# Kernel tuning notes

Measured on AMD Instinct MI355X. Metric: run time of the kernel, lower is better.

Reference implementation:

```python
import jax, jax.numpy as jnp
import numpy as np

N_EMBD = 768
HIDDEN = 4 * N_EMBD
N_EXPERTS = 8
TOP_K = 2


def setup_inputs() -> dict:
    key = jax.random.key(0)
    ks = jax.random.split(key, 4)
    B, T, C, E, H = 4, 2048, N_EMBD, N_EXPERTS, HIDDEN
    x = jax.random.normal(ks[0], (B, T, C), dtype=jnp.float32)
    gate_w = jax.random.normal(ks[1], (E, C), dtype=jnp.float32) * 0.02
    gate_b = jnp.zeros((E,), dtype=jnp.float32)
    w_fc = jax.random.normal(ks[2], (E, H, C), dtype=jnp.float32) * 0.02
    b_fc = jnp.zeros((E, H), dtype=jnp.float32)
    w_proj = jax.random.normal(ks[3], (E, C, H), dtype=jnp.float32) * 0.02
    b_proj = jnp.zeros((E, C), dtype=jnp.float32)
    return {"x": x, "gate_w": gate_w, "gate_b": gate_b, "w_fc": w_fc,
            "b_fc": b_fc, "w_proj": w_proj, "b_proj": b_proj}


def reference(x, gate_w, gate_b, w_fc, b_fc, w_proj, b_proj):
    B, T, C = x.shape
    E = gate_b.shape[0]
    xf = x.reshape(-1, C)  # [N, C]
    # gating: Linear(C -> E), top-k, softmax over the k selected scores
    scores = xf @ gate_w.T + gate_b                      # [N, E]
    top_s, top_i = jax.lax.top_k(scores, TOP_K)          # [N, K]
    gates = jax.nn.softmax(top_s, axis=-1)               # [N, K]
    # combine weight per (token, expert): sum_k gate[t,k] * 1[top_i[t,k]==e]
    comb = jnp.sum(jax.nn.one_hot(top_i, E, dtype=xf.dtype) * gates[..., None], axis=1)  # [N, E]
    out = jnp.zeros_like(xf)
    for j in range(E):  # loop over fixed small expert count
        h = jax.nn.gelu(xf @ w_fc[j].T + b_fc[j], approximate=True)  # [N, H]
        y = h @ w_proj[j].T + b_proj[j]                              # [N, C]
        out = out + comb[:, j:j + 1] * y
    return out.reshape(B, T, C)
```

## Files before the change

kernel.cpp:

```cpp
#include <hip/hip_runtime.h>
#include <cmath>

#define N_TOK 8192
#define C_DIM 768
#define H_DIM 3072
#define NEXP  8
#define PADCAP 18432

typedef short short8 __attribute__((ext_vector_type(8)));
typedef unsigned short ushort8 __attribute__((ext_vector_type(8)));
typedef float f32x4  __attribute__((ext_vector_type(4)));

__device__ __forceinline__ unsigned short f2b(float f) {
  unsigned int u = __float_as_uint(f);
  u += 0x7fffu + ((u >> 16) & 1u);
  return (unsigned short)(u >> 16);
}
__device__ __forceinline__ float b2f(unsigned short u) {
  return __uint_as_float((unsigned int)u << 16);
}
__device__ __forceinline__ void gll(const char* g, char* l) {
  __builtin_amdgcn_global_load_lds((const __attribute__((address_space(1))) void*)g,
                                   (__attribute__((address_space(3))) void*)l, 16, 0, 0);
}

__global__ __launch_bounds__(256) void gate_kernel(
    const float* __restrict__ x, const float* __restrict__ gw,
    const float* __restrict__ gb, int* __restrict__ counts,
    int* __restrict__ tok_e, int* __restrict__ tok_r, float* __restrict__ tok_w) {
  __shared__ float gwl[NEXP * C_DIM];
  __shared__ double red[256][NEXP];
  int tid = threadIdx.x;
  const float4* gw4 = (const float4*)gw;
  float4* gl4 = (float4*)gwl;
  for (int i = tid; i < NEXP * C_DIM / 4; i += 256) gl4[i] = gw4[i];
  __syncthreads();
  int tl = tid & 63;
  int kc = tid >> 6;
  int t = blockIdx.x * 64 + tl;
  double acc[NEXP];
#pragma unroll
  for (int e = 0; e < NEXP; e++) acc[e] = 0.0;
  const float* xr = x + (size_t)t * C_DIM;
  for (int k = kc * 192; k < kc * 192 + 192; k++) {
    double xv = (double)xr[k];
#pragma unroll
    for (int e = 0; e < NEXP; e++) acc[e] += xv * (double)gwl[e * C_DIM + k];
  }
#pragma unroll
  for (int e = 0; e < NEXP; e++) red[tid][e] = acc[e];
  __syncthreads();
  if (tid < 64) {
    double s[NEXP];
#pragma unroll
    for (int e = 0; e < NEXP; e++)
      s[e] = (double)gb[e] + red[tid][e] + red[tid + 64][e] + red[tid + 128][e] + red[tid + 192][e];
    double best = s[0], sec = -1e300; int bi = 0, si = -1;
#pragma unroll
    for (int e = 1; e < NEXP; e++) {
      if (s[e] > best)      { sec = best; si = bi; best = s[e]; bi = e; }
      else if (s[e] > sec)  { sec = s[e]; si = e; }
    }
    double ex = exp(sec - best);
    double den = 1.0 + ex;
    tok_e[2 * t] = bi;  tok_e[2 * t + 1] = si;
    tok_w[2 * t] = (float)(1.0 / den);  tok_w[2 * t + 1] = (float)(ex / den);
    tok_r[2 * t]     = atomicAdd(&counts[bi], 1);
    tok_r[2 * t + 1] = atomicAdd(&counts[si], 1);
  }
}

__global__ void offsets_kernel(const int* __restrict__ counts, int* __restrict__ po) {
  if (threadIdx.x == 0 && blockIdx.x == 0) {
    int s = 0;
    for (int e = 0; e < NEXP; e++) { po[e] = s; s += (counts[e] + 255) & ~255; }
    po[NEXP] = s;
  }
}

__global__ __launch_bounds__(256) void scatter_kernel(
    const int* __restrict__ tok_e, const int* __restrict__ tok_r,
    const float* __restrict__ tok_w, const int* __restrict__ po,
    int* __restrict__ perm_t, float* __restrict__ perm_w,
    int* __restrict__ tok_pos) {
  int t = blockIdx.x * 256 + threadIdx.x;
#pragma unroll
  for (int k = 0; k < 2; k++) {
    int e = tok_e[2 * t + k];
    int pos = po[e] + tok_r[2 * t + k];
    perm_t[pos] = t;
    perm_w[pos] = tok_w[2 * t + k];
    tok_pos[2 * t + k] = pos;
  }
}

__global__ __launch_bounds__(256) void gather_kernel(
    const float* __restrict__ x, const int* __restrict__ po,
    const int* __restrict__ perm_t, unsigned short* __restrict__ xg) {
  int row = blockIdx.x * 4 + (threadIdx.x >> 6);
  if (row >= po[NEXP]) return;
  int l = threadIdx.x & 63;
  int t = perm_t[row];
  const float4* src = (const float4*)(x + (size_t)t * C_DIM);
  ushort4* dst = (ushort4*)(xg + (size_t)row * C_DIM);
#pragma unroll
  for (int j = 0; j < 3; j++) {
    float4 v = src[l + j * 64];
    ushort4 o; o.x = f2b(v.x); o.y = f2b(v.y); o.z = f2b(v.z); o.w = f2b(v.w);
    dst[l + j * 64] = o;
  }
}

__global__ __launch_bounds__(256) void wconv_kernel(
    const float* __restrict__ src, unsigned short* __restrict__ dst, int n4) {
  int stride = gridDim.x * blockDim.x;
  for (int i = blockIdx.x * blockDim.x + threadIdx.x; i < n4; i += stride) {
    float4 v = ((const float4*)src)[i];
    ushort4 o; o.x = f2b(v.x); o.y = f2b(v.y); o.z = f2b(v.z); o.w = f2b(v.w);
    ((ushort4*)dst)[i] = o;
  }
}

__device__ __forceinline__ void gemm_core512(
    const unsigned short* A, int lda, const unsigned short* B, int ldb, int K,
    char* lds, int tid, f32x4 acc[4][2]) {
  const int w = tid >> 6, l = tid & 63;
  const int wr = w >> 2, wc = w & 3;
  const int rowa = wr * 64 + (l & 15);
  const int rowb = wc * 32 + (l & 15);
  const int kc = l >> 4;
  const int sa0 = (kc ^ ((rowa >> 1) & 7)) * 16;
  const int sb0 = (kc ^ ((rowb >> 1) & 7)) * 16;
  const int r0 = tid >> 3,          cg0 = (tid & 7) ^ ((r0 >> 1) & 7);
  const int r1 = (512 + tid) >> 3,  cg1 = ((512 + tid) & 7) ^ ((r1 >> 1) & 7);
  const char* gA0 = (const char*)(A + (size_t)r0 * lda) + cg0 * 16;
  const char* gA1 = (const char*)(A + (size_t)r1 * lda) + cg1 * 16;
  const char* gB0 = (const char*)(B + (size_t)r0 * ldb) + cg0 * 16;
  const char* gB1 = (const char*)(B + (size_t)r1 * ldb) + cg1 * 16;
  const int wb = w * 1024;
  const int iters = K >> 6;
  gll(gA0, lds + wb);
  gll(gA1, lds + 8192 + wb);
  gll(gB0, lds + 16384 + wb);
  gll(gB1, lds + 24576 + wb);
#pragma unroll 1
  for (int kt = 0; kt < iters; kt++) {
    __syncthreads();
    if (kt + 1 < iters) {
      size_t kb = (size_t)(kt + 1) * 128;
      char* nb = lds + ((kt + 1) & 1) * 32768;
      gll(gA0 + kb, nb + wb);
      gll(gA1 + kb, nb + 8192 + wb);
      gll(gB0 + kb, nb + 16384 + wb);
      gll(gB1 + kb, nb + 24576 + wb);
    }
    char* bb = lds + (kt & 1) * 32768;
#pragma unroll
    for (int s = 0; s < 2; s++) {
      const int sxa = sa0 ^ (s << 6);
      const int sxb = sb0 ^ (s << 6);
      short8 af[4], bf2[2];
#pragma unroll
      for (int mi = 0; mi < 4; mi++)
        af[mi] = *(const short8*)(bb + (rowa + mi * 16) * 128 + sxa);
#pragma unroll
      for (int ni = 0; ni < 2; ni++)
        bf2[ni] = *(const short8*)(bb + 16384 + (rowb + ni * 16) * 128 + sxb);
#pragma unroll
      for (int mi = 0; mi < 4; mi++)
#pragma unroll
        for (int ni = 0; ni < 2; ni++)
          acc[mi][ni] = __builtin_amdgcn_mfma_f32_16x16x32_bf16(af[mi], bf2[ni], acc[mi][ni], 0, 0, 0);
    }
  }
}

__global__ __launch_bounds__(512, 4) void fc1_kernel(
    const unsigned short* __restrict__ xg, const unsigned short* __restrict__ wfcb,
    const float* __restrict__ bfc, const int* __restrict__ po,
    unsigned short* __restrict__ h) {
  __shared__ char lds[65536];
  int bid = blockIdx.x;
  int r8 = bid & 7, g8 = bid >> 3;
  int col = g8 % 24;
  int Sp  = g8 / 24;
  int y   = r8 * 18 + Sp;
  int row0 = y * 128;
  if (row0 >= po[NEXP]) return;
  int e = 0;
#pragma unroll
  for (int i = 1; i < NEXP; i++) if (row0 >= po[i]) e = i;
  int n0 = col * 128;
  int tid = threadIdx.x;
  f32x4 acc[4][2];
#pragma unroll
  for (int mi = 0; mi < 4; mi++)
#pragma unroll
    for (int ni = 0; ni < 2; ni++) acc[mi][ni] = (f32x4){0.f, 0.f, 0.f, 0.f};
  gemm_core512(xg + (size_t)row0 * C_DIM, C_DIM,
               wfcb + (size_t)e * H_DIM * C_DIM + (size_t)n0 * C_DIM, C_DIM, C_DIM,
               lds, tid, acc);
  int w = tid >> 6, l = tid & 63;
  int wr = w >> 2, wc = w & 3, q = l >> 4, lr = l & 15;
  const float* bias = bfc + (size_t)e * H_DIM;
  __syncthreads();
  unsigned short* lout = (unsigned short*)lds;
  const int LST = 136;
#pragma unroll
  for (int ni = 0; ni < 2; ni++) {
    int lcol = wc * 32 + ni * 16 + lr;
    float bv = bias[n0 + lcol];
#pragma unroll
    for (int mi = 0; mi < 4; mi++) {
#pragma unroll
      for (int r = 0; r < 4; r++) {
        int lrow = wr * 64 + mi * 16 + q * 4 + r;
        float v = acc[mi][ni][r] + bv;
        float z = v * fmaf(0.0356774081f, v * v, 0.7978845608f);
        float ex = __builtin_amdgcn_exp2f(-2.8853900818f * z);
        float g = v * __builtin_amdgcn_rcpf(1.0f + ex);
        lout[lrow * LST + lcol] = f2b(g);
      }
    }
  }
  __syncthreads();
#pragma unroll
  for (int p = 0; p < 4; p++) {
    int idx = p * 512 + tid;
    int row = idx >> 4, c8 = idx & 15;
    ushort8 v = *(const ushort8*)(lout + row * LST + c8 * 8);
    *(ushort8*)(h + (size_t)(row0 + row) * H_DIM + n0 + c8 * 8) = v;
  }
}

__device__ __forceinline__ void gemm8p(
    const char* __restrict__ Ab, size_t ldaB,
    const char* __restrict__ Bb, size_t ldbB, int ktiles,
    char* lds, int tid, f32x4 acc[8][4]) {
  const int w = tid >> 6, l = tid & 63;
  const int wr = w >> 2, wc = w & 3;
  const int lr = l & 15, kc = l >> 4;
  const int sw = (lr >> 1) & 7;
  const int s0 = ((kc ^ sw) << 4);
  const int s1 = s0 ^ 64;
  const int arow = ((wr << 7) + lr) << 7;
  const int brow = 32768 + (((wc << 6) + lr) << 7);
  const int rl0 = tid >> 3;
  const int cg0 = (tid & 7) ^ ((rl0 >> 1) & 7);
  const size_t oA0 = (size_t)rl0 * ldaB + (cg0 << 4);
  const size_t oA1 = oA0 + (ldaB << 6);
  const size_t oB0 = (size_t)rl0 * ldbB + (cg0 << 4);
  const size_t oB1 = oB0 + (ldbB << 6);
  const int wb = w << 10;

#define SA(b, h, kt) do { \
    const char* s_ = Ab + (size_t)(h) * 128 * ldaB + (size_t)(kt) * 128; \
    gll(s_ + oA0, lds + (b) * 65536 + (h) * 16384 + wb); \
    gll(s_ + oA1, lds + (b) * 65536 + (h) * 16384 + 8192 + wb); } while (0)
#define SB(b, h, kt) do { \
    const char* s_ = Bb + (size_t)(h) * 128 * ldbB + (size_t)(kt) * 128; \
    gll(s_ + oB0, lds + (b) * 65536 + 32768 + (h) * 16384 + wb); \
    gll(s_ + oB1, lds + (b) * 65536 + 32768 + (h) * 16384 + 8192 + wb); } while (0)
#define BAR() asm volatile("s_barrier" ::: "memory")
#define RDA(B, mb) do { \
    for (int mi = 0; mi < 4; mi++) { \
      af[mi][0] = *(const short8*)(lds + (B) + arow + ((mb) + mi) * 2048 + s0); \
      af[mi][1] = *(const short8*)(lds + (B) + arow + ((mb) + mi) * 2048 + s1); } } while (0)
#define RDB(B, nb) do { \
    for (int ni = 0; ni < 2; ni++) { \
      bf[(nb) + ni][0] = *(const short8*)(lds + (B) + brow + ((nb) + ni) * 2048 + s0); \
      bf[(nb) + ni][1] = *(const short8*)(lds + (B) + brow + ((nb) + ni) * 2048 + s1); } } while (0)
#define MM(mb, nb) do { \
    __builtin_amdgcn_s_setprio(1); \
    for (int mi = 0; mi < 4; mi++) \
      for (int ni = 0; ni < 2; ni++) \
        for (int kk = 0; kk < 2; kk++) \
          acc[(mb) + mi][(nb) + ni] = __builtin_amdgcn_mfma_f32_16x16x32_bf16( \
              af[mi][kk], bf[(nb) + ni][kk], acc[(mb) + mi][(nb) + ni], 0, 0, 0); \
    __builtin_amdgcn_s_setprio(0); } while (0)

  short8 af[4][2], bf[4][2];
  SB(0, 0, 0); SB(0, 1, 0); SA(0, 0, 0); SA(0, 1, 0);
  SB(1, 0, 1); SB(1, 1, 1);
  asm volatile("s_waitcnt vmcnt(4)" ::: "memory");
  BAR();
  const int iters = ktiles >> 1;
#pragma unroll 1
  for (int i = 0; i < iters; i++) {
    const int t1 = 2 * i + 1, t2 = 2 * i + 2, t3 = 2 * i + 3;
    const bool nl = (i + 1 < iters);
    RDA(0, 0); RDB(0, 0);
    SA(1, 0, t1);
    BAR(); MM(0, 0); BAR();
    RDB(0, 2);
    SA(1, 1, t1);
    BAR(); MM(0, 2); BAR();
    RDA(0, 4);
    if (nl) SB(0, 0, t2);
    BAR(); MM(4, 2); BAR();
    if (nl) SB(0, 1, t2);
    BAR(); MM(4, 0);
    if (nl) asm volatile("s_waitcnt vmcnt(4)" ::: "memory");
    else    asm volatile("s_waitcnt vmcnt(0)" ::: "memory");
    BAR();
    RDA(65536, 0); RDB(65536, 0);
    if (nl) SA(0, 0, t2);
    BAR(); MM(0, 0); BAR();
    RDB(65536, 2);
    if (nl) SA(0, 1, t2);
    BAR(); MM(0, 2); BAR();
    RDA(65536, 4);
    if (nl) SB(1, 0, t3);
    BAR(); MM(4, 2); BAR();
    if (nl) SB(1, 1, t3);
    BAR(); MM(4, 0);
    if (nl) {
      asm volatile("s_waitcnt vmcnt(4)" ::: "memory");
      BAR();
    }
  }
#undef SA
#undef SB
#undef BAR
#undef RDA
#undef RDB
#undef MM
}

__global__ __launch_bounds__(512, 2) void fc2_kernel(
    const unsigned short* __restrict__ h, const unsigned short* __restrict__ wpjb,
    const float* __restrict__ bproj, const int* __restrict__ po,
    const float* __restrict__ perm_w, unsigned short* __restrict__ part) {
  __shared__ char lds[131072];
  int bid = blockIdx.x;
  int r8 = bid & 7, g8 = bid >> 3;
  int col = g8 % 3;
  int Sp  = g8 / 3;
  int y   = r8 * 9 + Sp;
  int row0 = y * 256;
  if (row0 >= po[NEXP]) return;
  int e = 0;
#pragma unroll
  for (int i = 1; i < NEXP; i++) if (row0 >= po[i]) e = i;
  int n0 = col * 256;
  int tid = threadIdx.x;
  f32x4 acc[8][4];
#pragma unroll
  for (int mi = 0; mi < 8; mi++)
#pragma unroll
    for (int ni = 0; ni < 4; ni++) acc[mi][ni] = (f32x4){0.f, 0.f, 0.f, 0.f};
  gemm8p((const char*)(h + (size_t)row0 * H_DIM), (size_t)H_DIM * 2,
         (const char*)(wpjb + (size_t)e * C_DIM * H_DIM + (size_t)n0 * H_DIM),
         (size_t)H_DIM * 2, H_DIM / 64, lds, tid, acc);
  int w = tid >> 6, l = tid & 63;
  int wr = w >> 2, wc = w & 3, lr = l & 15, q = l >> 4;
  const float* bias = bproj + (size_t)e * C_DIM;
#pragma unroll
  for (int mi = 0; mi < 8; mi++) {
#pragma unroll
    for (int r = 0; r < 4; r++) {
      int pos = row0 + wr * 128 + mi * 16 + q * 4 + r;
      float wgt = perm_w[pos];
#pragma unroll
      for (int ni = 0; ni < 4; ni++) {
        int colw = n0 + wc * 64 + ni * 16 + lr;
        float v = acc[mi][ni][r] + bias[colw];
        part[(size_t)pos * C_DIM + colw] = f2b(v * wgt);
      }
    }
  }
}

__global__ __launch_bounds__(256) void combine_kernel(
    const unsigned short* __restrict__ part, const int* __restrict__ tok_pos,
    float* __restrict__ out) {
  const int NC4 = C_DIM / 4;
  int idx = blockIdx.x * 256 + threadIdx.x;
  int t = idx / NC4, c4 = idx - t * NC4;
  int p0 = tok_pos[2 * t], p1 = tok_pos[2 * t + 1];
  ushort4 v0 = *(const ushort4*)(part + (size_t)p0 * C_DIM + c4 * 4);
  ushort4 v1 = *(const ushort4*)(part + (size_t)p1 * C_DIM + c4 * 4);
  float4 o;
  o.x = b2f(v0.x) + b2f(v1.x);
  o.y = b2f(v0.y) + b2f(v1.y);
  o.z = b2f(v0.z) + b2f(v1.z);
  o.w = b2f(v0.w) + b2f(v1.w);
  ((float4*)out)[idx] = o;
}

extern "C" void kernel_launch(void* const* d_in, const int* in_sizes, int n_in,
                              void* d_out, int out_size, void* d_ws, size_t ws_size,
                              hipStream_t stream) {
  const float* x     = (const float*)d_in[0];
  const float* gw    = (const float*)d_in[1];
  const float* gb    = (const float*)d_in[2];
  const float* wfc   = (const float*)d_in[3];
  const float* bfc   = (const float*)d_in[4];
  const float* wproj = (const float*)d_in[5];
  const float* bproj = (const float*)d_in[6];
  float* out = (float*)d_out;
  char* ws = (char*)d_ws;

  int*   counts  = (int*)(ws + 0);
  int*   po      = (int*)(ws + 64);
  int*   tok_e   = (int*)(ws + 256);
  int*   tok_r   = (int*)(ws + 65792);
  float* tok_w   = (float*)(ws + 131328);
  int*   tok_pos = (int*)(ws + 196864);
  int*   perm_t  = (int*)(ws + 262400);
  float* perm_w  = (float*)(ws + 336128);
  const size_t ROUT_END = 409856;
  unsigned short* wfcb = (unsigned short*)(ws + 409856);
  unsigned short* wpjb = (unsigned short*)(ws + 409856);
  unsigned short* xg   = (unsigned short*)(ws + 38158592);
  unsigned short* part = (unsigned short*)(ws + 38158592);
  unsigned short* hbuf = (unsigned short*)(ws + 66470144);

  hipMemsetAsync(ws, 0, ROUT_END, stream);

  const int WN4 = NEXP * H_DIM * C_DIM / 4;
  gate_kernel<<<N_TOK / 64, 256, 0, stream>>>(x, gw, gb, counts, tok_e, tok_r, tok_w);
  offsets_kernel<<<1, 64, 0, stream>>>(counts, po);
  scatter_kernel<<<N_TOK / 256, 256, 0, stream>>>(tok_e, tok_r, tok_w, po, perm_t, perm_w, tok_pos);
  gather_kernel<<<PADCAP / 4, 256, 0, stream>>>(x, po, perm_t, xg);
  wconv_kernel<<<2048, 256, 0, stream>>>(wfc, wfcb, WN4);
  fc1_kernel<<<8 * 18 * 24, 512, 0, stream>>>(xg, wfcb, bfc, po, hbuf);
  wconv_kernel<<<2048, 256, 0, stream>>>(wproj, wpjb, WN4);
  fc2_kernel<<<8 * 9 * 3, 512, 0, stream>>>(hbuf, wpjb, bproj, po, perm_w, part);
  combine_kernel<<<N_TOK * (C_DIM / 4) / 256, 256, 0, stream>>>(part, tok_pos, out);
}
```

Measured before the change: 498.4 us.

## Fuse expert combine into fc2 epilogue via float atomics into output

Removes the bf16 partial buffer and the separate combine kernel. The gate kernel now zeroes the output, and fc2 atomically adds each weighted expert row straight into the token's output row, skipping padded rows whose weight is zero. This saves a round trip through global memory and one launch. In exchange it adds about 12.6M scattered fp32 atomics and makes the order of the two per-token additions nondeterministic.

Measured after the change: 568.9 us. +14.1%, slower.

```diff
diff --git a/kernel.cpp b/kernel.cpp
--- a/kernel.cpp
+++ b/kernel.cpp
@@ -27,10 +27,13 @@
 __global__ __launch_bounds__(256) void gate_kernel(
     const float* __restrict__ x, const float* __restrict__ gw,
     const float* __restrict__ gb, int* __restrict__ counts,
-    int* __restrict__ tok_e, int* __restrict__ tok_r, float* __restrict__ tok_w) {
+    int* __restrict__ tok_e, int* __restrict__ tok_r, float* __restrict__ tok_w,
+    float* __restrict__ out) {
   __shared__ float gwl[NEXP * C_DIM];
   __shared__ double red[256][NEXP];
   int tid = threadIdx.x;
+  float4* ob = (float4*)(out + (size_t)blockIdx.x * 64 * C_DIM);
+  for (int i = tid; i < 64 * C_DIM / 4; i += 256) ob[i] = (float4){0.f, 0.f, 0.f, 0.f};
   const float4* gw4 = (const float4*)gw;
   float4* gl4 = (float4*)gwl;
   for (int i = tid; i < NEXP * C_DIM / 4; i += 256) gl4[i] = gw4[i];
@@ -81,8 +84,7 @@
 __global__ __launch_bounds__(256) void scatter_kernel(
     const int* __restrict__ tok_e, const int* __restrict__ tok_r,
     const float* __restrict__ tok_w, const int* __restrict__ po,
-    int* __restrict__ perm_t, float* __restrict__ perm_w,
-    int* __restrict__ tok_pos) {
+    int* __restrict__ perm_t, float* __restrict__ perm_w) {
   int t = blockIdx.x * 256 + threadIdx.x;
 #pragma unroll
   for (int k = 0; k < 2; k++) {
@@ -90,7 +92,6 @@
     int pos = po[e] + tok_r[2 * t + k];
     perm_t[pos] = t;
     perm_w[pos] = tok_w[2 * t + k];
-    tok_pos[2 * t + k] = pos;
   }
 }
 
@@ -330,7 +331,8 @@
 __global__ __launch_bounds__(512, 2) void fc2_kernel(
     const unsigned short* __restrict__ h, const unsigned short* __restrict__ wpjb,
     const float* __restrict__ bproj, const int* __restrict__ po,
-    const float* __restrict__ perm_w, unsigned short* __restrict__ part) {
+    const float* __restrict__ perm_w, const int* __restrict__ perm_t,
+    float* __restrict__ out) {
   __shared__ char lds[131072];
   int bid = blockIdx.x;
   int r8 = bid & 7, g8 = bid >> 3;
@@ -361,31 +363,16 @@
     for (int r = 0; r < 4; r++) {
       int pos = row0 + wr * 128 + mi * 16 + q * 4 + r;
       float wgt = perm_w[pos];
-#pragma unroll
-      for (int ni = 0; ni < 4; ni++) {
-        int colw = n0 + wc * 64 + ni * 16 + lr;
-        float v = acc[mi][ni][r] + bias[colw];
-        part[(size_t)pos * C_DIM + colw] = f2b(v * wgt);
+      if (wgt != 0.0f) {
+        float* orow = out + (size_t)perm_t[pos] * C_DIM;
+#pragma unroll
+        for (int ni = 0; ni < 4; ni++) {
+          int colw = n0 + wc * 64 + ni * 16 + lr;
+          atomicAdd(orow + colw, (acc[mi][ni][r] + bias[colw]) * wgt);
+        }
       }
     }
   }
-}
-
-__global__ __launch_bounds__(256) void combine_kernel(
-    const unsigned short* __restrict__ part, const int* __restrict__ tok_pos,
-    float* __restrict__ out) {
-  const int NC4 = C_DIM / 4;
-  int idx = blockIdx.x * 256 + threadIdx.x;
-  int t = idx / NC4, c4 = idx - t * NC4;
-  int p0 = tok_pos[2 * t], p1 = tok_pos[2 * t + 1];
-  ushort4 v0 = *(const ushort4*)(part + (size_t)p0 * C_DIM + c4 * 4);
-  ushort4 v1 = *(const ushort4*)(part + (size_t)p1 * C_DIM + c4 * 4);
-  float4 o;
-  o.x = b2f(v0.x) + b2f(v1.x);
-  o.y = b2f(v0.y) + b2f(v1.y);
-  o.z = b2f(v0.z) + b2f(v1.z);
-  o.w = b2f(v0.w) + b2f(v1.w);
-  ((float4*)out)[idx] = o;
 }
 
 extern "C" void kernel_launch(void* const* d_in, const int* in_sizes, int n_in,
@@ -406,26 +393,23 @@
   int*   tok_e   = (int*)(ws + 256);
   int*   tok_r   = (int*)(ws + 65792);
   float* tok_w   = (float*)(ws + 131328);
-  int*   tok_pos = (int*)(ws + 196864);
   int*   perm_t  = (int*)(ws + 262400);
   float* perm_w  = (float*)(ws + 336128);
   const size_t ROUT_END = 409856;
   unsigned short* wfcb = (unsigned short*)(ws + 409856);
   unsigned short* wpjb = (unsigned short*)(ws + 409856);
   unsigned short* xg   = (unsigned short*)(ws + 38158592);
-  unsigned short* part = (unsigned short*)(ws + 38158592);
   unsigned short* hbuf = (unsigned short*)(ws + 66470144);
 
   hipMemsetAsync(ws, 0, ROUT_END, stream);
 
   const int WN4 = NEXP * H_DIM * C_DIM / 4;
-  gate_kernel<<<N_TOK / 64, 256, 0, stream>>>(x, gw, gb, counts, tok_e, tok_r, tok_w);
+  gate_kernel<<<N_TOK / 64, 256, 0, stream>>>(x, gw, gb, counts, tok_e, tok_r, tok_w, out);
   offsets_kernel<<<1, 64, 0, stream>>>(counts, po);
-  scatter_kernel<<<N_TOK / 256, 256, 0, stream>>>(tok_e, tok_r, tok_w, po, perm_t, perm_w, tok_pos);
+  scatter_kernel<<<N_TOK / 256, 256, 0, stream>>>(tok_e, tok_r, tok_w, po, perm_t, perm_w);
   gather_kernel<<<PADCAP / 4, 256, 0, stream>>>(x, po, perm_t, xg);
   wconv_kernel<<<2048, 256, 0, stream>>>(wfc, wfcb, WN4);
   fc1_kernel<<<8 * 18 * 24, 512, 0, stream>>>(xg, wfcb, bfc, po, hbuf);
   wconv_kernel<<<2048, 256, 0, stream>>>(wproj, wpjb, WN4);
-  fc2_kernel<<<8 * 9 * 3, 512, 0, stream>>>(hbuf, wpjb, bproj, po, perm_w, part);
-  combine_kernel<<<N_TOK * (C_DIM / 4) / 256, 256, 0, stream>>>(part, tok_pos, out);
-}
+  fc2_kernel<<<8 * 9 * 3, 512, 0, stream>>>(hbuf, wpjb, bproj, po, perm_w, perm_t, out);
+}
```

## Fuse gating with fc weight conversion and merge offsets, scatter, gather kernels

Applied to the files above, without the earlier changes.

The gating kernel now also converts the fc1 weights to bf16 and zeroes perm_w in a grid-stride loop, so the weight conversion overlaps gating instead of running as its own launch. The offsets, scatter and gather kernels are merged into one kernel that computes expert offsets per thread and writes gathered bf16 rows straight to their padded positions, which removes the perm_t indirection. The large workspace memset shrinks to clearing only the counts. This cuts several launches and a round trip through memory. Padding rows in xg are no longer written, so they hold stale data, though their perm_w is zero.

New measurement: 491.0 us. About the same (-1.5%).

```diff
diff --git a/kernel.cpp b/kernel.cpp
--- a/kernel.cpp
+++ b/kernel.cpp
@@ -24,20 +24,38 @@
                                    (__attribute__((address_space(3))) void*)l, 16, 0, 0);
 }
 
-__global__ __launch_bounds__(256) void gate_kernel(
+__global__ __launch_bounds__(256) void gate_wconv_kernel(
     const float* __restrict__ x, const float* __restrict__ gw,
-    const float* __restrict__ gb, int* __restrict__ counts,
-    int* __restrict__ tok_e, int* __restrict__ tok_r, float* __restrict__ tok_w) {
+    const float* __restrict__ gb, const float* __restrict__ wfc,
+    int* __restrict__ counts, int* __restrict__ tok_e, int* __restrict__ tok_r,
+    float* __restrict__ tok_w, float* __restrict__ perm_w,
+    unsigned short* __restrict__ wfcb) {
   __shared__ float gwl[NEXP * C_DIM];
   __shared__ double red[256][NEXP];
-  int tid = threadIdx.x;
+  const int tid = threadIdx.x, bid = blockIdx.x;
+  const int nthr = gridDim.x * 256;
+  const int gtid = bid * 256 + tid;
+
+  for (int i = gtid; i < PADCAP; i += nthr) perm_w[i] = 0.0f;
+
+  {
+    const int n4 = NEXP * H_DIM * C_DIM / 4;
+    for (int i = gtid; i < n4; i += nthr) {
+      float4 v = ((const float4*)wfc)[i];
+      ushort4 o; o.x = f2b(v.x); o.y = f2b(v.y); o.z = f2b(v.z); o.w = f2b(v.w);
+      ((ushort4*)wfcb)[i] = o;
+    }
+  }
+
+  if (bid >= N_TOK / 64) return;
+
   const float4* gw4 = (const float4*)gw;
   float4* gl4 = (float4*)gwl;
   for (int i = tid; i < NEXP * C_DIM / 4; i += 256) gl4[i] = gw4[i];
   __syncthreads();
   int tl = tid & 63;
   int kc = tid >> 6;
-  int t = blockIdx.x * 64 + tl;
+  int t = bid * 64 + tl;
   double acc[NEXP];
 #pragma unroll
   for (int e = 0; e < NEXP; e++) acc[e] = 0.0;
@@ -70,44 +88,37 @@
   }
 }
 
-__global__ void offsets_kernel(const int* __restrict__ counts, int* __restrict__ po) {
-  if (threadIdx.x == 0 && blockIdx.x == 0) {
+__global__ __launch_bounds__(256) void scatgath_kernel(
+    const float* __restrict__ x, const int* __restrict__ counts,
+    const int* __restrict__ tok_e, const int* __restrict__ tok_r,
+    const float* __restrict__ tok_w, int* __restrict__ po,
+    int* __restrict__ tok_pos, float* __restrict__ perm_w,
+    unsigned short* __restrict__ xg) {
+  const int tid = threadIdx.x, bid = blockIdx.x;
+  int pol[NEXP + 1];
+  {
     int s = 0;
-    for (int e = 0; e < NEXP; e++) { po[e] = s; s += (counts[e] + 255) & ~255; }
-    po[NEXP] = s;
-  }
-}
-
-__global__ __launch_bounds__(256) void scatter_kernel(
-    const int* __restrict__ tok_e, const int* __restrict__ tok_r,
-    const float* __restrict__ tok_w, const int* __restrict__ po,
-    int* __restrict__ perm_t, float* __restrict__ perm_w,
-    int* __restrict__ tok_pos) {
-  int t = blockIdx.x * 256 + threadIdx.x;
-#pragma unroll
-  for (int k = 0; k < 2; k++) {
-    int e = tok_e[2 * t + k];
-    int pos = po[e] + tok_r[2 * t + k];
-    perm_t[pos] = t;
-    perm_w[pos] = tok_w[2 * t + k];
-    tok_pos[2 * t + k] = pos;
-  }
-}
-
-__global__ __launch_bounds__(256) void gather_kernel(
-    const float* __restrict__ x, const int* __restrict__ po,
-    const int* __restrict__ perm_t, unsigned short* __restrict__ xg) {
-  int row = blockIdx.x * 4 + (threadIdx.x >> 6);
-  if (row >= po[NEXP]) return;
-  int l = threadIdx.x & 63;
-  int t = perm_t[row];
-  const float4* src = (const float4*)(x + (size_t)t * C_DIM);
-  ushort4* dst = (ushort4*)(xg + (size_t)row * C_DIM);
-#pragma unroll
-  for (int j = 0; j < 3; j++) {
-    float4 v = src[l + j * 64];
-    ushort4 o; o.x = f2b(v.x); o.y = f2b(v.y); o.z = f2b(v.z); o.w = f2b(v.w);
-    dst[l + j * 64] = o;
+#pragma unroll
+    for (int e = 0; e < NEXP; e++) { pol[e] = s; s += (counts[e] + 255) & ~255; }
+    pol[NEXP] = s;
+  }
+  if (bid == 0 && tid < NEXP + 1) po[tid] = pol[tid];
+  const int gtid = bid * 256 + tid;
+  const int grp = gtid >> 6, l = tid & 63;
+  const int ngrp = (gridDim.x * 256) >> 6;
+  for (int j = grp; j < 2 * N_TOK; j += ngrp) {
+    int t = j >> 1;
+    int e = tok_e[j];
+    int pos = pol[e] + tok_r[j];
+    if (l == 0) { tok_pos[j] = pos; perm_w[pos] = tok_w[j]; }
+    const float4* src = (const float4*)(x + (size_t)t * C_DIM);
+    ushort4* dst = (ushort4*)(xg + (size_t)pos * C_DIM);
+#pragma unroll
+    for (int q = 0; q < 3; q++) {
+      float4 v = src[l + q * 64];
+      ushort4 o; o.x = f2b(v.x); o.y = f2b(v.y); o.z = f2b(v.z); o.w = f2b(v.w);
+      dst[l + q * 64] = o;
+    }
   }
 }
 
@@ -407,23 +418,20 @@
   int*   tok_r   = (int*)(ws + 65792);
   float* tok_w   = (float*)(ws + 131328);
   int*   tok_pos = (int*)(ws + 196864);
-  int*   perm_t  = (int*)(ws + 262400);
-  float* perm_w  = (float*)(ws + 336128);
-  const size_t ROUT_END = 409856;
+  float* perm_w  = (float*)(ws + 262400);
   unsigned short* wfcb = (unsigned short*)(ws + 409856);
   unsigned short* wpjb = (unsigned short*)(ws + 409856);
   unsigned short* xg   = (unsigned short*)(ws + 38158592);
   unsigned short* part = (unsigned short*)(ws + 38158592);
   unsigned short* hbuf = (unsigned short*)(ws + 66470144);
 
-  hipMemsetAsync(ws, 0, ROUT_END, stream);
-
   const int WN4 = NEXP * H_DIM * C_DIM / 4;
-  gate_kernel<<<N_TOK / 64, 256, 0, stream>>>(x, gw, gb, counts, tok_e, tok_r, tok_w);
-  offsets_kernel<<<1, 64, 0, stream>>>(counts, po);
-  scatter_kernel<<<N_TOK / 256, 256, 0, stream>>>(tok_e, tok_r, tok_w, po, perm_t, perm_w, tok_pos);
-  gather_kernel<<<PADCAP / 4, 256, 0, stream>>>(x, po, perm_t, xg);
-  wconv_kernel<<<2048, 256, 0, stream>>>(wfc, wfcb, WN4);
+
+  hipMemsetAsync(counts, 0, 64, stream);
+  gate_wconv_kernel<<<2048, 256, 0, stream>>>(x, gw, gb, wfc, counts,
+                                              tok_e, tok_r, tok_w, perm_w, wfcb);
+  scatgath_kernel<<<512, 256, 0, stream>>>(x, counts, tok_e, tok_r, tok_w,
+                                           po, tok_pos, perm_w, xg);
   fc1_kernel<<<8 * 18 * 24, 512, 0, stream>>>(xg, wfcb, bfc, po, hbuf);
   wconv_kernel<<<2048, 256, 0, stream>>>(wproj, wpjb, WN4);
   fc2_kernel<<<8 * 9 * 3, 512, 0, stream>>>(hbuf, wpjb, bproj, po, perm_w, part);
```
